# Optimization experiments

Measured on AMD Instinct MI355X. Metric: run time of the kernel, lower is better.

Reference implementation:

```python
import jax, jax.numpy as jnp
import numpy as np
import math

N = 384      # group/table size -> W is [N, N, N]
R = 8        # tensor-ring bond dimension
B = 524288   # number of (j, k) index pairs to look up


def setup_inputs() -> dict:
    key = jax.random.key(0)
    k1, k2, k3, k4 = jax.random.split(key, 4)
    # Tensor_Layer init: init_scale**(1/depth) * randn(siz) / sqrt(siz[0]), init_scale=1, siz[0]=R
    s = 1.0 / math.sqrt(R)
    A = jax.random.normal(k1, (R, N, R), dtype=jnp.float32) * s
    Bf = jax.random.normal(k2, (R, N, R), dtype=jnp.float32) * s
    C = jax.random.normal(k3, (R, N, R), dtype=jnp.float32) * s
    x = jax.random.randint(k4, (B, 2), 0, N, dtype=jnp.int32)
    return {"A": A, "Bf": Bf, "C": C, "x": x}


def reference(A, Bf, C, x):
    # net_Weight: full tensor-ring reconstruction of W[i,j,k] (materialized, as in original)
    W = jnp.einsum('aib,bjc,cka->ijk', A, Bf, C)  # [N, N, N]
    # index_select: flatten last two dims, gather at x0*N + x1, transpose -> [B, N]
    # equivalently out[b, i] = W[i, x[b,0], x[b,1]]
    out = W[:, x[:, 0], x[:, 1]].T  # [B, N]
    return out
```

## Files before the change

### kernel.cpp

```cpp
#include <hip/hip_runtime.h>

#define NN 384
#define RR 8
#define NR (NN * RR)
#define IPAD 385
#define GSTR 72

typedef _Float16 half4v __attribute__((ext_vector_type(4)));
typedef _Float16 half8v __attribute__((ext_vector_type(8)));
typedef float f32x4 __attribute__((ext_vector_type(4)));

__global__ __launch_bounds__(512, 4)
void dtn_mfma16(const float* __restrict__ A, const float* __restrict__ Bf,
                const float* __restrict__ C, const int* __restrict__ x,
                float* __restrict__ out)
{
    __shared__ __align__(16) _Float16 A2c[8 * IPAD * 8];
    __shared__ __align__(16) _Float16 Gh[64 * GSTR];

    const int t = threadIdx.x;
    const long b0 = (long)blockIdx.x * 256;

    #pragma unroll
    for (int it = 0; it < 6; ++it) {
        const int idx = t + it * 512;
        const int i = idx >> 3;
        const int a = idx & 7;
        const float4* src = reinterpret_cast<const float4*>(A + (size_t)a * NR + (size_t)i * RR);
        const float4 f0 = src[0];
        const float4 f1 = src[1];
        half8v h;
        h[0] = (_Float16)f0.x; h[1] = (_Float16)f0.y; h[2] = (_Float16)f0.z; h[3] = (_Float16)f0.w;
        h[4] = (_Float16)f1.x; h[5] = (_Float16)f1.y; h[6] = (_Float16)f1.z; h[7] = (_Float16)f1.w;
        *reinterpret_cast<half8v*>(&A2c[(size_t)(a * IPAD + i) * 8]) = h;
    }

    const int lane = t & 63;
    const int w    = t >> 6;
    const int mt   = w & 3;
    const int nh   = w >> 2;
    const int a16  = lane & 15;
    const int q    = lane >> 4;

    #pragma unroll 1
    for (int bt = 0; bt < 4; ++bt) {
        __syncthreads();

        {
            const int bl = t >> 3;
            const int a  = t & 7;
            const long pair = b0 + bt * 64 + bl;
            const int j = x[2 * pair];
            const int k = x[2 * pair + 1];
            const float* Bj = Bf + (size_t)j * RR;
            const float* Ck = C + (size_t)k * RR + a;
            float ck[8];
            #pragma unroll
            for (int c = 0; c < 8; ++c)
                ck[c] = Ck[(size_t)c * NR];
            half8v h;
            #pragma unroll
            for (int b2 = 0; b2 < 8; ++b2) {
                const float4* br = reinterpret_cast<const float4*>(Bj + (size_t)b2 * NR);
                const float4 r0 = br[0];
                const float4 r1 = br[1];
                const float s = r0.x * ck[0] + r0.y * ck[1] + r0.z * ck[2] + r0.w * ck[3]
                              + r1.x * ck[4] + r1.y * ck[5] + r1.z * ck[6] + r1.w * ck[7];
                h[b2] = (_Float16)s;
            }
            *reinterpret_cast<half8v*>(&Gh[bl * GSTR + a * 8]) = h;
        }
        __syncthreads();

        const half4v af0 = *reinterpret_cast<const half4v*>(&Gh[(mt * 16 + a16) * GSTR +  0 + 4 * q]);
        const half4v af1 = *reinterpret_cast<const half4v*>(&Gh[(mt * 16 + a16) * GSTR + 16 + 4 * q]);
        const half4v af2 = *reinterpret_cast<const half4v*>(&Gh[(mt * 16 + a16) * GSTR + 32 + 4 * q]);
        const half4v af3 = *reinterpret_cast<const half4v*>(&Gh[(mt * 16 + a16) * GSTR + 48 + 4 * q]);

        const long prow0 = b0 + bt * 64 + mt * 16 + 4 * q;

        #pragma unroll 2
        for (int nt = 0; nt < 12; ++nt) {
            const int n0 = nh * 192 + nt * 16;
            const int col = n0 + a16;
            f32x4 acc = {0.f, 0.f, 0.f, 0.f};
            const half4v bf0 = *reinterpret_cast<const half4v*>(
                &A2c[(size_t)((0 + (q >> 1)) * IPAD + col) * 8 + 4 * (q & 1)]);
            acc = __builtin_amdgcn_mfma_f32_16x16x16f16(af0, bf0, acc, 0, 0, 0);
            const half4v bf1 = *reinterpret_cast<const half4v*>(
                &A2c[(size_t)((2 + (q >> 1)) * IPAD + col) * 8 + 4 * (q & 1)]);
            acc = __builtin_amdgcn_mfma_f32_16x16x16f16(af1, bf1, acc, 0, 0, 0);
            const half4v bf2 = *reinterpret_cast<const half4v*>(
                &A2c[(size_t)((4 + (q >> 1)) * IPAD + col) * 8 + 4 * (q & 1)]);
            acc = __builtin_amdgcn_mfma_f32_16x16x16f16(af2, bf2, acc, 0, 0, 0);
            const half4v bf3 = *reinterpret_cast<const half4v*>(
                &A2c[(size_t)((6 + (q >> 1)) * IPAD + col) * 8 + 4 * (q & 1)]);
            acc = __builtin_amdgcn_mfma_f32_16x16x16f16(af3, bf3, acc, 0, 0, 0);

            float* op = out + (size_t)prow0 * NN + col;
            op[0]            = acc[0];
            op[(size_t)NN]   = acc[1];
            op[(size_t)2*NN] = acc[2];
            op[(size_t)3*NN] = acc[3];
        }
    }
}

extern "C" void kernel_launch(void* const* d_in, const int* in_sizes, int n_in,
                              void* d_out, int out_size, void* d_ws, size_t ws_size,
                              hipStream_t stream) {
    const float* A  = (const float*)d_in[0];
    const float* Bf = (const float*)d_in[1];
    const float* C  = (const float*)d_in[2];
    const int*   x  = (const int*)d_in[3];
    float* out = (float*)d_out;
    const int B = in_sizes[3] / 2;
    dtn_mfma16<<<B / 256, 512, 0, stream>>>(A, Bf, C, x, out);
}
```

Measured before the change: 179.8 us.

## Split output columns across two blocks to halve LDS footprint

Each block now handles only half of the 384 output columns, staging just the corresponding half of A in shared memory. The grid doubles and launch bounds request more resident blocks per CU, aiming at higher occupancy to better hide memory latency on the output stores. In exchange, the per-pair G computation and the index loads are duplicated across the two half-blocks.

```diff
diff --git a/kernel.cpp b/kernel.cpp
--- a/kernel.cpp
+++ b/kernel.cpp
@@ -3,42 +3,44 @@
 #define NN 384
 #define RR 8
 #define NR (NN * RR)
-#define IPAD 385
+#define IPADH 193
 #define GSTR 72
 
 typedef _Float16 half4v __attribute__((ext_vector_type(4)));
 typedef _Float16 half8v __attribute__((ext_vector_type(8)));
 typedef float f32x4 __attribute__((ext_vector_type(4)));
 
-__global__ __launch_bounds__(512, 4)
-void dtn_mfma16(const float* __restrict__ A, const float* __restrict__ Bf,
-                const float* __restrict__ C, const int* __restrict__ x,
-                float* __restrict__ out)
+__global__ __launch_bounds__(512, 8)
+void dtn_mfma16h(const float* __restrict__ A, const float* __restrict__ Bf,
+                 const float* __restrict__ C, const int* __restrict__ x,
+                 float* __restrict__ out)
 {
-    __shared__ __align__(16) _Float16 A2c[8 * IPAD * 8];
+    __shared__ __align__(16) _Float16 A2c[8 * IPADH * 8];
     __shared__ __align__(16) _Float16 Gh[64 * GSTR];
 
-    const int t = threadIdx.x;
-    const long b0 = (long)blockIdx.x * 256;
+    const int t  = threadIdx.x;
+    const int pbk = blockIdx.x >> 1;
+    const int ih  = blockIdx.x & 1;
+    const long b0 = (long)pbk * 256;
 
     #pragma unroll
-    for (int it = 0; it < 6; ++it) {
-        const int idx = t + it * 512;
-        const int i = idx >> 3;
-        const int a = idx & 7;
-        const float4* src = reinterpret_cast<const float4*>(A + (size_t)a * NR + (size_t)i * RR);
+    for (int it = 0; it < 3; ++it) {
+        const int L = it * 512 + t;
+        const int c = L / 192;
+        const int il = L - c * 192;
+        const float4* src = reinterpret_cast<const float4*>(A) + 2 * (c * NN + ih * 192 + il);
         const float4 f0 = src[0];
         const float4 f1 = src[1];
         half8v h;
         h[0] = (_Float16)f0.x; h[1] = (_Float16)f0.y; h[2] = (_Float16)f0.z; h[3] = (_Float16)f0.w;
         h[4] = (_Float16)f1.x; h[5] = (_Float16)f1.y; h[6] = (_Float16)f1.z; h[7] = (_Float16)f1.w;
-        *reinterpret_cast<half8v*>(&A2c[(size_t)(a * IPAD + i) * 8]) = h;
+        *reinterpret_cast<half8v*>(&A2c[(size_t)(c * IPADH + il) * 8]) = h;
     }
 
     const int lane = t & 63;
     const int w    = t >> 6;
     const int mt   = w & 3;
-    const int nh   = w >> 2;
+    const int nh2  = w >> 2;
     const int a16  = lane & 15;
     const int q    = lane >> 4;
 
@@ -80,24 +82,24 @@
         const long prow0 = b0 + bt * 64 + mt * 16 + 4 * q;
 
         #pragma unroll 2
-        for (int nt = 0; nt < 12; ++nt) {
-            const int n0 = nh * 192 + nt * 16;
-            const int col = n0 + a16;
+        for (int nt = 0; nt < 6; ++nt) {
+            const int il = nh2 * 96 + nt * 16 + a16;
+            const int colg = ih * 192 + il;
             f32x4 acc = {0.f, 0.f, 0.f, 0.f};
             const half4v bf0 = *reinterpret_cast<const half4v*>(
-                &A2c[(size_t)((0 + (q >> 1)) * IPAD + col) * 8 + 4 * (q & 1)]);
+                &A2c[(size_t)((0 + (q >> 1)) * IPADH + il) * 8 + 4 * (q & 1)]);
             acc = __builtin_amdgcn_mfma_f32_16x16x16f16(af0, bf0, acc, 0, 0, 0);
             const half4v bf1 = *reinterpret_cast<const half4v*>(
-                &A2c[(size_t)((2 + (q >> 1)) * IPAD + col) * 8 + 4 * (q & 1)]);
+                &A2c[(size_t)((2 + (q >> 1)) * IPADH + il) * 8 + 4 * (q & 1)]);
             acc = __builtin_amdgcn_mfma_f32_16x16x16f16(af1, bf1, acc, 0, 0, 0);
             const half4v bf2 = *reinterpret_cast<const half4v*>(
-                &A2c[(size_t)((4 + (q >> 1)) * IPAD + col) * 8 + 4 * (q & 1)]);
+                &A2c[(size_t)((4 + (q >> 1)) * IPADH + il) * 8 + 4 * (q & 1)]);
             acc = __builtin_amdgcn_mfma_f32_16x16x16f16(af2, bf2, acc, 0, 0, 0);
             const half4v bf3 = *reinterpret_cast<const half4v*>(
-                &A2c[(size_t)((6 + (q >> 1)) * IPAD + col) * 8 + 4 * (q & 1)]);
+                &A2c[(size_t)((6 + (q >> 1)) * IPADH + il) * 8 + 4 * (q & 1)]);
             acc = __builtin_amdgcn_mfma_f32_16x16x16f16(af3, bf3, acc, 0, 0, 0);
 
-            float* op = out + (size_t)prow0 * NN + col;
+            float* op = out + (size_t)prow0 * NN + colg;
             op[0]            = acc[0];
             op[(size_t)NN]   = acc[1];
             op[(size_t)2*NN] = acc[2];
@@ -115,5 +117,5 @@
     const int*   x  = (const int*)d_in[3];
     float* out = (float*)d_out;
     const int B = in_sizes[3] / 2;
-    dtn_mfma16<<<B / 256, 512, 0, stream>>>(A, Bf, C, x, out);
+    dtn_mfma16h<<<(B / 256) * 2, 512, 0, stream>>>(A, Bf, C, x, out);
 }
```

New measurement: 201.7 us. +12.2%, slower.

## Make each wave own its 16 pairs to drop per-tile block barriers

Applied to the files above, without the earlier changes.

Each wave now builds its own 16-row G tile in a private shared-memory slice and computes all 384 output columns for it. This removes the four-iteration loop with two block-wide barriers per tile; only one barrier remains, after the A staging. Blocks now cover 128 pairs instead of 256, so the grid doubles and the fp16 conversion of A into shared memory is repeated twice as often per output row. Each lane also computes two a-values of G, using float2 loads of C.

```diff
diff --git a/kernel.cpp b/kernel.cpp
--- a/kernel.cpp
+++ b/kernel.cpp
@@ -11,15 +11,15 @@
 typedef float f32x4 __attribute__((ext_vector_type(4)));
 
 __global__ __launch_bounds__(512, 4)
-void dtn_mfma16(const float* __restrict__ A, const float* __restrict__ Bf,
-                const float* __restrict__ C, const int* __restrict__ x,
-                float* __restrict__ out)
+void dtn_mfma16w(const float* __restrict__ A, const float* __restrict__ Bf,
+                 const float* __restrict__ C, const int* __restrict__ x,
+                 float* __restrict__ out)
 {
     __shared__ __align__(16) _Float16 A2c[8 * IPAD * 8];
-    __shared__ __align__(16) _Float16 Gh[64 * GSTR];
+    __shared__ __align__(16) _Float16 Gh[8 * 16 * GSTR];
 
     const int t = threadIdx.x;
-    const long b0 = (long)blockIdx.x * 256;
+    const long b0 = (long)blockIdx.x * 128;
 
     #pragma unroll
     for (int it = 0; it < 6; ++it) {
@@ -34,75 +34,73 @@
         h[4] = (_Float16)f1.x; h[5] = (_Float16)f1.y; h[6] = (_Float16)f1.z; h[7] = (_Float16)f1.w;
         *reinterpret_cast<half8v*>(&A2c[(size_t)(a * IPAD + i) * 8]) = h;
     }
+    __syncthreads();
 
     const int lane = t & 63;
     const int w    = t >> 6;
-    const int mt   = w & 3;
-    const int nh   = w >> 2;
-    const int a16  = lane & 15;
-    const int q    = lane >> 4;
+    _Float16* Ghw  = &Gh[w * 16 * GSTR];
 
-    #pragma unroll 1
-    for (int bt = 0; bt < 4; ++bt) {
-        __syncthreads();
+    {
+        const int bl = lane >> 2;
+        const int a0 = (lane & 3) * 2;
+        const long pair = b0 + w * 16 + bl;
+        const int j = x[2 * pair];
+        const int k = x[2 * pair + 1];
+        const float* Bj = Bf + (size_t)j * RR;
+        const float* Ck = C + (size_t)k * RR + a0;
+        float2 ck[8];
+        #pragma unroll
+        for (int c = 0; c < 8; ++c)
+            ck[c] = *reinterpret_cast<const float2*>(Ck + (size_t)c * NR);
+        half8v h0, h1;
+        #pragma unroll
+        for (int b2 = 0; b2 < 8; ++b2) {
+            const float4* br = reinterpret_cast<const float4*>(Bj + (size_t)b2 * NR);
+            const float4 r0 = br[0];
+            const float4 r1 = br[1];
+            const float s0 = r0.x * ck[0].x + r0.y * ck[1].x + r0.z * ck[2].x + r0.w * ck[3].x
+                           + r1.x * ck[4].x + r1.y * ck[5].x + r1.z * ck[6].x + r1.w * ck[7].x;
+            const float s1 = r0.x * ck[0].y + r0.y * ck[1].y + r0.z * ck[2].y + r0.w * ck[3].y
+                           + r1.x * ck[4].y + r1.y * ck[5].y + r1.z * ck[6].y + r1.w * ck[7].y;
+            h0[b2] = (_Float16)s0;
+            h1[b2] = (_Float16)s1;
+        }
+        *reinterpret_cast<half8v*>(&Ghw[bl * GSTR + a0 * 8]) = h0;
+        *reinterpret_cast<half8v*>(&Ghw[bl * GSTR + a0 * 8 + 8]) = h1;
+    }
 
-        {
-            const int bl = t >> 3;
-            const int a  = t & 7;
-            const long pair = b0 + bt * 64 + bl;
-            const int j = x[2 * pair];
-            const int k = x[2 * pair + 1];
-            const float* Bj = Bf + (size_t)j * RR;
-            const float* Ck = C + (size_t)k * RR + a;
-            float ck[8];
-            #pragma unroll
-            for (int c = 0; c < 8; ++c)
-                ck[c] = Ck[(size_t)c * NR];
-            half8v h;
-            #pragma unroll
-            for (int b2 = 0; b2 < 8; ++b2) {
-                const float4* br = reinterpret_cast<const float4*>(Bj + (size_t)b2 * NR);
-                const float4 r0 = br[0];
-                const float4 r1 = br[1];
-                const float s = r0.x * ck[0] + r0.y * ck[1] + r0.z * ck[2] + r0.w * ck[3]
-                              + r1.x * ck[4] + r1.y * ck[5] + r1.z * ck[6] + r1.w * ck[7];
-                h[b2] = (_Float16)s;
-            }
-            *reinterpret_cast<half8v*>(&Gh[bl * GSTR + a * 8]) = h;
-        }
-        __syncthreads();
+    const int a16 = lane & 15;
+    const int q   = lane >> 4;
 
-        const half4v af0 = *reinterpret_cast<const half4v*>(&Gh[(mt * 16 + a16) * GSTR +  0 + 4 * q]);
-        const half4v af1 = *reinterpret_cast<const half4v*>(&Gh[(mt * 16 + a16) * GSTR + 16 + 4 * q]);
-        const half4v af2 = *reinterpret_cast<const half4v*>(&Gh[(mt * 16 + a16) * GSTR + 32 + 4 * q]);
-        const half4v af3 = *reinterpret_cast<const half4v*>(&Gh[(mt * 16 + a16) * GSTR + 48 + 4 * q]);
+    const half4v af0 = *reinterpret_cast<const half4v*>(&Ghw[a16 * GSTR +  0 + 4 * q]);
+    const half4v af1 = *reinterpret_cast<const half4v*>(&Ghw[a16 * GSTR + 16 + 4 * q]);
+    const half4v af2 = *reinterpret_cast<const half4v*>(&Ghw[a16 * GSTR + 32 + 4 * q]);
+    const half4v af3 = *reinterpret_cast<const half4v*>(&Ghw[a16 * GSTR + 48 + 4 * q]);
 
-        const long prow0 = b0 + bt * 64 + mt * 16 + 4 * q;
+    const long prow0 = b0 + w * 16 + 4 * q;
 
-        #pragma unroll 2
-        for (int nt = 0; nt < 12; ++nt) {
-            const int n0 = nh * 192 + nt * 16;
-            const int col = n0 + a16;
-            f32x4 acc = {0.f, 0.f, 0.f, 0.f};
-            const half4v bf0 = *reinterpret_cast<const half4v*>(
-                &A2c[(size_t)((0 + (q >> 1)) * IPAD + col) * 8 + 4 * (q & 1)]);
-            acc = __builtin_amdgcn_mfma_f32_16x16x16f16(af0, bf0, acc, 0, 0, 0);
-            const half4v bf1 = *reinterpret_cast<const half4v*>(
-                &A2c[(size_t)((2 + (q >> 1)) * IPAD + col) * 8 + 4 * (q & 1)]);
-            acc = __builtin_amdgcn_mfma_f32_16x16x16f16(af1, bf1, acc, 0, 0, 0);
-            const half4v bf2 = *reinterpret_cast<const half4v*>(
-                &A2c[(size_t)((4 + (q >> 1)) * IPAD + col) * 8 + 4 * (q & 1)]);
-            acc = __builtin_amdgcn_mfma_f32_16x16x16f16(af2, bf2, acc, 0, 0, 0);
-            const half4v bf3 = *reinterpret_cast<const half4v*>(
-                &A2c[(size_t)((6 + (q >> 1)) * IPAD + col) * 8 + 4 * (q & 1)]);
-            acc = __builtin_amdgcn_mfma_f32_16x16x16f16(af3, bf3, acc, 0, 0, 0);
+    #pragma unroll 2
+    for (int nt = 0; nt < 24; ++nt) {
+        const int col = nt * 16 + a16;
+        f32x4 acc = {0.f, 0.f, 0.f, 0.f};
+        const half4v bf0 = *reinterpret_cast<const half4v*>(
+            &A2c[(size_t)((0 + (q >> 1)) * IPAD + col) * 8 + 4 * (q & 1)]);
+        acc = __builtin_amdgcn_mfma_f32_16x16x16f16(af0, bf0, acc, 0, 0, 0);
+        const half4v bf1 = *reinterpret_cast<const half4v*>(
+            &A2c[(size_t)((2 + (q >> 1)) * IPAD + col) * 8 + 4 * (q & 1)]);
+        acc = __builtin_amdgcn_mfma_f32_16x16x16f16(af1, bf1, acc, 0, 0, 0);
+        const half4v bf2 = *reinterpret_cast<const half4v*>(
+            &A2c[(size_t)((4 + (q >> 1)) * IPAD + col) * 8 + 4 * (q & 1)]);
+        acc = __builtin_amdgcn_mfma_f32_16x16x16f16(af2, bf2, acc, 0, 0, 0);
+        const half4v bf3 = *reinterpret_cast<const half4v*>(
+            &A2c[(size_t)((6 + (q >> 1)) * IPAD + col) * 8 + 4 * (q & 1)]);
+        acc = __builtin_amdgcn_mfma_f32_16x16x16f16(af3, bf3, acc, 0, 0, 0);
 
-            float* op = out + (size_t)prow0 * NN + col;
-            op[0]            = acc[0];
-            op[(size_t)NN]   = acc[1];
-            op[(size_t)2*NN] = acc[2];
-            op[(size_t)3*NN] = acc[3];
-        }
+        float* op = out + (size_t)prow0 * NN + col;
+        op[0]            = acc[0];
+        op[(size_t)NN]   = acc[1];
+        op[(size_t)2*NN] = acc[2];
+        op[(size_t)3*NN] = acc[3];
     }
 }
 
@@ -115,5 +113,5 @@
     const int*   x  = (const int*)d_in[3];
     float* out = (float*)d_out;
     const int B = in_sizes[3] / 2;
-    dtn_mfma16<<<B / 256, 512, 0, stream>>>(A, Bf, C, x, out);
+    dtn_mfma16w<<<B / 128, 512, 0, stream>>>(A, Bf, C, x, out);
 }
```

Result: faster. 164.8 us (median of 2 runs) (-8.3%).
